# Kernel optimization log

Hardware: AMD Instinct MI355X
Metric: run time of the kernel (lower is better)

Reference implementation:

```python
import jax, jax.numpy as jnp
import numpy as np

B, T, D, N = 16, 4096, 512, 3


def _window_sum(x, k):
    # x: [B, T, ...] -> sliding-window sum of size k, stride 1 -> [B, T-k+1, ...]
    c = jnp.cumsum(x, axis=1)
    c = jnp.concatenate([jnp.zeros_like(c[:, :1]), c], axis=1)
    return c[:, k:] - c[:, :-k]


def setup_inputs() -> dict:
    key = jax.random.key(0)
    ks = jax.random.split(key, 7)
    s_prev = jax.random.normal(ks[0], (B, D), jnp.float32)
    enc_hs = jax.random.normal(ks[1], (B, T, D), jnp.float32)
    # realistic padding mask: True = padded position
    lengths = jax.random.randint(ks[2], (B,), T // 2, T + 1)
    src_mask = jnp.arange(T)[None, :] >= lengths[:, None]
    scale = 1.0 / np.sqrt(D)
    Vw = jax.random.normal(ks[3], (N, D, D), jnp.float32) * scale
    Vb = jax.random.normal(ks[4], (N, D), jnp.float32) * 0.01
    Ww = jax.random.normal(ks[5], (N, D, D), jnp.float32) * scale
    Wb = jax.random.normal(ks[6], (N, D), jnp.float32) * 0.01
    return {"s_prev": s_prev, "enc_hs": enc_hs, "src_mask": src_mask,
            "Vw": Vw, "Vb": Vb, "Ww": Ww, "Wb": Wb}


def _level(s_prev, hs, mask, vw, vb, ww, wb):
    # hs: [B, L, D], mask: [B, L] (True = masked)
    # torch Linear: y = x @ W^T + b, weight is [out, in]
    v = jnp.einsum('bld,ed->ble', hs, vw) + vb            # V_i(hs)
    att = jnp.einsum('bd,bld->bl', s_prev, v)             # bmm(s_prev, V(hs)^T)
    att = jnp.where(mask, -jnp.inf, att)
    att = jax.nn.softmax(att, axis=-1)                    # [B, L]
    pooled = jnp.einsum('bl,bld->bd', att, hs)            # bmm(att, hs)
    ctx = pooled @ ww.T + wb                              # W_i(.)
    return ctx, att


def reference(s_prev, enc_hs, src_mask, Vw, Vb, Ww, Wb):
    ctx, att = _level(s_prev, enc_hs, src_mask, Vw[0], Vb[0], Ww[0], Wb[0])
    for i in range(1, N):
        k = i + 1
        hs_ngram = _window_sum(enc_hs, k) / k                      # AvgPool1d(k,1)
        n_mask = _window_sum(src_mask.astype(jnp.float32), k) > 0  # any masked in window
        c, _ = _level(s_prev, hs_ngram, n_mask, Vw[i], Vb[i], Ww[i], Wb[i])
        ctx = ctx + c
    return ctx, att
```

## Files before the change

### kernel.cpp

```cpp
#include <hip/hip_runtime.h>

#define BB 16
#define TT 4096
#define DD 512
#define CH 32
#define NY (TT/CH)
#define NEG (-1.0e30f)

#define OFF_Q     64
#define OFF_P0    (OFF_Q + 3*BB*DD)
#define OFF_M     (OFF_P0 + BB*TT)
#define OFF_S     (OFF_M + 3*BB*NY)
#define OFF_MT    (OFF_S + 3*BB*NY)
#define OFF_TOT   (OFF_MT + 64)
#define OFF_PART  (OFF_TOT + 64)
#define OFF_POOL  (OFF_PART + 3*NY*BB*DD)

__global__ void __launch_bounds__(256) k_lengths(const unsigned char* __restrict__ mask,
                                                 int* __restrict__ lengths) {
    __shared__ int sflag;
    __shared__ int wsum[4];
    const int tid = threadIdx.x;
    const int b = blockIdx.x;
    if (tid == 0) sflag = 0;
    __syncthreads();
    const uint4* m4 = (const uint4*)mask;
    int f = 0;
    #pragma unroll 4
    for (int idx = tid; idx < BB * TT / 16; idx += 256) {
        const uint4 w = m4[idx];
        f |= (((w.x | w.y | w.z | w.w) & 0xFFFFFF00u) != 0u);
    }
    if (f) atomicOr(&sflag, 1);
    __syncthreads();
    const bool byte_layout = (sflag != 0);
    const int* m32 = (const int*)mask;
    int cnt = 0;
    if (byte_layout) {
        for (int t = tid; t < TT; t += 256) cnt += (mask[b * TT + t] != 0);
    } else {
        for (int t = tid; t < TT; t += 256) cnt += (m32[b * TT + t] != 0);
    }
    #pragma unroll
    for (int m = 32; m >= 1; m >>= 1) cnt += __shfl_xor(cnt, m, 64);
    if ((tid & 63) == 0) wsum[tid >> 6] = cnt;
    __syncthreads();
    if (tid == 0) lengths[b] = TT - (wsum[0] + wsum[1] + wsum[2] + wsum[3]);
}

__global__ void __launch_bounds__(1024) k_q(const float* __restrict__ s_prev,
                                            const float* __restrict__ Vw,
                                            float* __restrict__ q) {
    __shared__ float red[4][DD];
    const int ib = blockIdx.x;
    const int b = ib % BB;
    const int i = ib / BB;
    const int ec = threadIdx.x >> 8;
    const int d0 = threadIdx.x & 255;
    const float* sp = s_prev + b * DD + ec * 128;
    const float* W = Vw + (size_t)i * DD * DD + (size_t)(ec * 128) * DD;
    float a0 = 0.f, a1 = 0.f;
    #pragma unroll 4
    for (int e = 0; e < 128; e++) {
        const float se = sp[e];
        a0 += se * W[e * DD + d0];
        a1 += se * W[e * DD + d0 + 256];
    }
    red[ec][d0] = a0;
    red[ec][d0 + 256] = a1;
    __syncthreads();
    if (threadIdx.x < DD)
        q[(size_t)ib * DD + threadIdx.x] = red[0][threadIdx.x] + red[1][threadIdx.x]
                                         + red[2][threadIdx.x] + red[3][threadIdx.x];
}

__global__ void __launch_bounds__(512, 4) k_fused(const float* __restrict__ enc,
                                                  const float* __restrict__ q,
                                                  const int* __restrict__ lengths,
                                                  float* __restrict__ p0,
                                                  float* __restrict__ mbuf,
                                                  float* __restrict__ sbuf,
                                                  float* __restrict__ part) {
    __shared__ float se[CH + 2][DD];
    __shared__ float sp[CH + 2][3];
    __shared__ float su[3][CH];
    const int b = blockIdx.x;
    const int y = blockIdx.y;
    const int t0 = y * CH;
    const int len = lengths[b];
    const int tid = threadIdx.x;
    if (t0 >= len) {
        if (tid < 3) {
            mbuf[(size_t)(tid * BB + b) * NY + y] = NEG;
            sbuf[(size_t)(tid * BB + b) * NY + y] = 0.f;
        }
        return;
    }
    const int wv = tid >> 6, lane = tid & 63;

    const float4* q40 = (const float4*)(q + (size_t)(0 * BB + b) * DD);
    const float4* q41 = (const float4*)(q + (size_t)(1 * BB + b) * DD);
    const float4* q42 = (const float4*)(q + (size_t)(2 * BB + b) * DD);
    const float4 qa0 = q40[lane], qb0 = q40[64 + lane];
    const float4 qa1 = q41[lane], qb1 = q41[64 + lane];
    const float4 qa2 = q42[lane], qb2 = q42[64 + lane];

    auto row_task = [&](const int r, const bool wp0) {
        const int t = t0 + r;
        float4 x0 = make_float4(0.f, 0.f, 0.f, 0.f), x1 = x0;
        if (t < TT) {
            const float4* e4 = (const float4*)(enc + ((size_t)b * TT + t) * DD);
            x0 = e4[lane]; x1 = e4[64 + lane];
        }
        ((float4*)se[r])[lane] = x0;
        ((float4*)se[r])[64 + lane] = x1;
        float d0 = x0.x*qa0.x + x0.y*qa0.y + x0.z*qa0.z + x0.w*qa0.w
                 + x1.x*qb0.x + x1.y*qb0.y + x1.z*qb0.z + x1.w*qb0.w;
        float d1 = x0.x*qa1.x + x0.y*qa1.y + x0.z*qa1.z + x0.w*qa1.w
                 + x1.x*qb1.x + x1.y*qb1.y + x1.z*qb1.z + x1.w*qb1.w;
        float d2 = x0.x*qa2.x + x0.y*qa2.y + x0.z*qa2.z + x0.w*qa2.w
                 + x1.x*qb2.x + x1.y*qb2.y + x1.z*qb2.z + x1.w*qb2.w;
        #pragma unroll
        for (int m = 32; m >= 1; m >>= 1) {
            d0 += __shfl_xor(d0, m, 64);
            d1 += __shfl_xor(d1, m, 64);
            d2 += __shfl_xor(d2, m, 64);
        }
        if (lane == 0) {
            sp[r][0] = d0; sp[r][1] = d1; sp[r][2] = d2;
            if (wp0 && t < TT) p0[(size_t)b * TT + t] = d0;
        }
    };
    #pragma unroll
    for (int rr = 0; rr < 4; rr++) row_task(wv + rr * 8, true);
    if (wv < 2) row_task(CH + wv, false);
    __syncthreads();

    if (tid < 192) {
        const int i = wv;
        const bool act = lane < CH;
        const int r = lane & (CH - 1);
        const int l = t0 + r;
        const bool valid = act && (l < (len - i));
        float v = NEG;
        if (act) {
            float s = sp[r][i];
            if (i > 0) s += sp[r + 1][i];
            if (i > 1) s += sp[r + 2][i];
            const float kin = (i == 0) ? 1.0f : ((i == 1) ? 0.5f : (1.0f / 3.0f));
            v = valid ? s * kin : NEG;
        }
        float m = v;
        #pragma unroll
        for (int mm = 32; mm >= 1; mm >>= 1) m = fmaxf(m, __shfl_xor(m, mm, 64));
        const float u = valid ? __expf(v - m) : 0.f;
        if (act) su[i][r] = u;
        float ts = u;
        #pragma unroll
        for (int mm = 32; mm >= 1; mm >>= 1) ts += __shfl_xor(ts, mm, 64);
        if (lane == 0) {
            mbuf[(size_t)(i * BB + b) * NY + y] = m;
            sbuf[(size_t)(i * BB + b) * NY + y] = ts;
        }
    }
    __syncthreads();

    float va = se[0][tid], vb2 = se[1][tid];
    float a0 = 0.f, a1 = 0.f, a2 = 0.f;
    #pragma unroll
    for (int g = 0; g < CH / 4; g++) {
        const float4 U0 = *(const float4*)&su[0][g * 4];
        const float4 U1 = *(const float4*)&su[1][g * 4];
        const float4 U2 = *(const float4*)&su[2][g * 4];
        const float u0a[4] = {U0.x, U0.y, U0.z, U0.w};
        const float u1a[4] = {U1.x, U1.y, U1.z, U1.w};
        const float u2a[4] = {U2.x, U2.y, U2.z, U2.w};
        #pragma unroll
        for (int j = 0; j < 4; j++) {
            const float vc = se[g * 4 + j + 2][tid];
            const float w1 = va + vb2;
            const float w2 = w1 + vc;
            a0 += u0a[j] * va;
            a1 += u1a[j] * w1;
            a2 += u2a[j] * w2;
            va = vb2; vb2 = vc;
        }
    }
    a1 *= 0.5f; a2 *= (1.0f / 3.0f);
    float* pt = part + (size_t)y * BB * DD + (size_t)b * DD + tid;
    pt[0] = a0;
    pt[(size_t)NY * BB * DD] = a1;
    pt[(size_t)2 * NY * BB * DD] = a2;
}

__global__ void __launch_bounds__(256) k_reduce(const float* __restrict__ part,
                                                const float* __restrict__ mbuf,
                                                const float* __restrict__ sbuf,
                                                float* __restrict__ pooled,
                                                float* __restrict__ mtot,
                                                float* __restrict__ tot) {
    __shared__ float ssc[NY];
    const int blk = blockIdx.x;
    const int ib = blk >> 1;
    const int d = ((blk & 1) << 8) + threadIdx.x;
    const int i = ib / BB, b = ib % BB;
    if (threadIdx.x < 64) {
        const int lane = threadIdx.x;
        float ml[2], sl[2];
        float m = NEG;
        #pragma unroll
        for (int j = 0; j < 2; j++) {
            ml[j] = mbuf[(size_t)ib * NY + lane * 2 + j];
            sl[j] = sbuf[(size_t)ib * NY + lane * 2 + j];
            m = fmaxf(m, ml[j]);
        }
        #pragma unroll
        for (int s = 32; s >= 1; s >>= 1) m = fmaxf(m, __shfl_xor(m, s, 64));
        float t = 0.f;
        #pragma unroll
        for (int j = 0; j < 2; j++) t += sl[j] * __expf(ml[j] - m);
        #pragma unroll
        for (int s = 32; s >= 1; s >>= 1) t += __shfl_xor(t, s, 64);
        const float inv = 1.0f / t;
        #pragma unroll
        for (int j = 0; j < 2; j++)
            ssc[lane * 2 + j] = __expf(ml[j] - m) * inv;
        if (lane == 0 && (blk & 1) == 0) { mtot[ib] = m; tot[ib] = t; }
    }
    __syncthreads();
    const float* base = part + (size_t)i * NY * BB * DD + (size_t)b * DD + d;
    float s = 0.f;
    #pragma unroll 8
    for (int yy = 0; yy < NY; yy++) s += base[(size_t)yy * BB * DD] * ssc[yy];
    pooled[(size_t)ib * DD + d] = s;
}

__global__ void __launch_bounds__(256) k_out(const float* __restrict__ pooled,
                                             const float* __restrict__ Ww,
                                             const float* __restrict__ Wb,
                                             const float* __restrict__ p0,
                                             const int* __restrict__ lengths,
                                             const float* __restrict__ mtot,
                                             const float* __restrict__ tot,
                                             float* __restrict__ ctx,
                                             float* __restrict__ att) {
    if (blockIdx.x < BB * DD / 4) {
        const int wid = blockIdx.x * 4 + (threadIdx.x >> 6);
        const int lane = threadIdx.x & 63;
        const int b = wid >> 9;
        const int e = wid & 511;
        float acc = 0.f;
        #pragma unroll
        for (int i = 0; i < 3; i++) {
            const float4* pr = (const float4*)(pooled + (size_t)(i * BB + b) * DD);
            const float4* wr = (const float4*)(Ww + ((size_t)i * DD + e) * DD);
            const float4 pA = pr[lane], pB = pr[64 + lane];
            const float4 wA = wr[lane], wB = wr[64 + lane];
            acc += pA.x * wA.x + pA.y * wA.y + pA.z * wA.z + pA.w * wA.w
                 + pB.x * wB.x + pB.y * wB.y + pB.z * wB.z + pB.w * wB.w;
        }
        #pragma unroll
        for (int m = 32; m >= 1; m >>= 1) acc += __shfl_xor(acc, m, 64);
        if (lane == 0)
            ctx[(size_t)b * DD + e] = acc + Wb[e] + Wb[DD + e] + Wb[2 * DD + e];
    } else {
        const int idx = (blockIdx.x - BB * DD / 4) * 256 + threadIdx.x;
        const int b = idx >> 12;
        const int t = idx & (TT - 1);
        att[idx] = (t < lengths[b]) ? __expf(p0[idx] - mtot[b]) * (1.0f / tot[b]) : 0.f;
    }
}

extern "C" void kernel_launch(void* const* d_in, const int* in_sizes, int n_in,
                              void* d_out, int out_size, void* d_ws, size_t ws_size,
                              hipStream_t stream) {
    const float* s_prev = (const float*)d_in[0];
    const float* enc    = (const float*)d_in[1];
    const void*  mask   = d_in[2];
    const float* Vw     = (const float*)d_in[3];
    const float* Ww     = (const float*)d_in[5];
    const float* Wb     = (const float*)d_in[6];

    float* out = (float*)d_out;
    float* ctx = out;
    float* att = out + BB * DD;

    float* W       = (float*)d_ws;
    int*   lengths = (int*)d_ws;
    float* q       = W + OFF_Q;
    float* p0      = W + OFF_P0;
    float* mbuf    = W + OFF_M;
    float* sbuf    = W + OFF_S;
    float* mtot    = W + OFF_MT;
    float* tot     = W + OFF_TOT;
    float* part    = W + OFF_PART;
    float* pooled  = W + OFF_POOL;

    k_lengths<<<BB, 256, 0, stream>>>((const unsigned char*)mask, lengths);
    k_q<<<48, 1024, 0, stream>>>(s_prev, Vw, q);
    k_fused<<<dim3(BB, NY), 512, 0, stream>>>(enc, q, lengths, p0, mbuf, sbuf, part);
    k_reduce<<<96, 256, 0, stream>>>(part, mbuf, sbuf, pooled, mtot, tot);
    k_out<<<BB * DD / 4 + BB * TT / 256, 256, 0, stream>>>(pooled, Ww, Wb, p0, lengths,
                                                           mtot, tot, ctx, att);
}
```

Baseline: 251.3 us.

## Process four chunks per block with online softmax and split q projection

Each fused block now walks four consecutive 32-row chunks and merges their partial softmax statistics and weighted sums with an online rescale. This cuts the number of per-chunk partials written to and read back from global memory by four, and shrinks the reduction kernel's work. The q projection is split across many more blocks, merged into the length kernel, with a small extra kernel to sum the pieces, so more CUs work on that stage. The trade-offs are fewer fused blocks (less parallelism and poorer tail balance), one extra launch, and extra barriers inside each block.

```diff
diff --git a/kernel.cpp b/kernel.cpp
--- a/kernel.cpp
+++ b/kernel.cpp
@@ -4,74 +4,94 @@
 #define TT 4096
 #define DD 512
 #define CH 32
-#define NY (TT/CH)
+#define GR 4
+#define NG (TT/(CH*GR))
 #define NEG (-1.0e30f)
 
 #define OFF_Q     64
-#define OFF_P0    (OFF_Q + 3*BB*DD)
+#define OFF_QP    (OFF_Q + 3*BB*DD)
+#define OFF_P0    (OFF_QP + 8*3*BB*DD)
 #define OFF_M     (OFF_P0 + BB*TT)
-#define OFF_S     (OFF_M + 3*BB*NY)
-#define OFF_MT    (OFF_S + 3*BB*NY)
+#define OFF_S     (OFF_M + 3*BB*NG)
+#define OFF_MT    (OFF_S + 3*BB*NG)
 #define OFF_TOT   (OFF_MT + 64)
 #define OFF_PART  (OFF_TOT + 64)
-#define OFF_POOL  (OFF_PART + 3*NY*BB*DD)
-
-__global__ void __launch_bounds__(256) k_lengths(const unsigned char* __restrict__ mask,
-                                                 int* __restrict__ lengths) {
-    __shared__ int sflag;
-    __shared__ int wsum[4];
+#define OFF_POOL  (OFF_PART + 3*NG*BB*DD)
+
+__global__ void __launch_bounds__(256) k_pre(const unsigned char* __restrict__ mask,
+                                             const float* __restrict__ s_prev,
+                                             const float* __restrict__ Vw,
+                                             int* __restrict__ lengths,
+                                             float* __restrict__ qpart) {
     const int tid = threadIdx.x;
-    const int b = blockIdx.x;
-    if (tid == 0) sflag = 0;
-    __syncthreads();
-    const uint4* m4 = (const uint4*)mask;
-    int f = 0;
-    #pragma unroll 4
-    for (int idx = tid; idx < BB * TT / 16; idx += 256) {
-        const uint4 w = m4[idx];
-        f |= (((w.x | w.y | w.z | w.w) & 0xFFFFFF00u) != 0u);
-    }
-    if (f) atomicOr(&sflag, 1);
-    __syncthreads();
-    const bool byte_layout = (sflag != 0);
-    const int* m32 = (const int*)mask;
-    int cnt = 0;
-    if (byte_layout) {
-        for (int t = tid; t < TT; t += 256) cnt += (mask[b * TT + t] != 0);
+    if (blockIdx.x < BB) {
+        __shared__ int sflag;
+        __shared__ int wsum[4];
+        const int b = blockIdx.x;
+        if (tid == 0) sflag = 0;
+        __syncthreads();
+        const uint4* m4 = (const uint4*)mask;
+        int f = 0;
+        #pragma unroll 4
+        for (int idx = tid; idx < BB * TT / 16; idx += 256) {
+            const uint4 w = m4[idx];
+            f |= (((w.x | w.y | w.z | w.w) & 0xFFFFFF00u) != 0u);
+        }
+        if (f) atomicOr(&sflag, 1);
+        __syncthreads();
+        const bool byte_layout = (sflag != 0);
+        const int* m32 = (const int*)mask;
+        int cnt = 0;
+        if (byte_layout) {
+            for (int t = tid; t < TT; t += 256) cnt += (mask[b * TT + t] != 0);
+        } else {
+            for (int t = tid; t < TT; t += 256) cnt += (m32[b * TT + t] != 0);
+        }
+        #pragma unroll
+        for (int m = 32; m >= 1; m >>= 1) cnt += __shfl_xor(cnt, m, 64);
+        if ((tid & 63) == 0) wsum[tid >> 6] = cnt;
+        __syncthreads();
+        if (tid == 0) lengths[b] = TT - (wsum[0] + wsum[1] + wsum[2] + wsum[3]);
     } else {
-        for (int t = tid; t < TT; t += 256) cnt += (m32[b * TT + t] != 0);
-    }
+        __shared__ float4 red[2][128];
+        const int idx = blockIdx.x - BB;
+        const int ib = idx >> 3;
+        const int ec = idx & 7;
+        const int b = ib % BB;
+        const int i = ib / BB;
+        const int es = tid >> 7;
+        const int dq = tid & 127;
+        const int e0 = ec * 64 + es * 32;
+        const float* sp = s_prev + b * DD + e0;
+        const float4* W = (const float4*)(Vw + (size_t)i * DD * DD + (size_t)e0 * DD) + dq;
+        float4 acc = make_float4(0.f, 0.f, 0.f, 0.f);
+        #pragma unroll 8
+        for (int e = 0; e < 32; e++) {
+            const float sev = sp[e];
+            const float4 w = W[e * 128];
+            acc.x += sev * w.x; acc.y += sev * w.y;
+            acc.z += sev * w.z; acc.w += sev * w.w;
+        }
+        red[es][dq] = acc;
+        __syncthreads();
+        if (tid < 128) {
+            const float4 r0 = red[0][tid], r1 = red[1][tid];
+            const float4 o = make_float4(r0.x + r1.x, r0.y + r1.y,
+                                         r0.z + r1.z, r0.w + r1.w);
+            ((float4*)(qpart + (size_t)idx * DD))[tid] = o;
+        }
+    }
+}
+
+__global__ void __launch_bounds__(256) k_q2(const float* __restrict__ qpart,
+                                            float* __restrict__ q) {
+    const int idx = blockIdx.x * 256 + threadIdx.x;
+    const int ib = idx / DD;
+    const int d = idx % DD;
+    float s = 0.f;
     #pragma unroll
-    for (int m = 32; m >= 1; m >>= 1) cnt += __shfl_xor(cnt, m, 64);
-    if ((tid & 63) == 0) wsum[tid >> 6] = cnt;
-    __syncthreads();
-    if (tid == 0) lengths[b] = TT - (wsum[0] + wsum[1] + wsum[2] + wsum[3]);
-}
-
-__global__ void __launch_bounds__(1024) k_q(const float* __restrict__ s_prev,
-                                            const float* __restrict__ Vw,
-                                            float* __restrict__ q) {
-    __shared__ float red[4][DD];
-    const int ib = blockIdx.x;
-    const int b = ib % BB;
-    const int i = ib / BB;
-    const int ec = threadIdx.x >> 8;
-    const int d0 = threadIdx.x & 255;
-    const float* sp = s_prev + b * DD + ec * 128;
-    const float* W = Vw + (size_t)i * DD * DD + (size_t)(ec * 128) * DD;
-    float a0 = 0.f, a1 = 0.f;
-    #pragma unroll 4
-    for (int e = 0; e < 128; e++) {
-        const float se = sp[e];
-        a0 += se * W[e * DD + d0];
-        a1 += se * W[e * DD + d0 + 256];
-    }
-    red[ec][d0] = a0;
-    red[ec][d0 + 256] = a1;
-    __syncthreads();
-    if (threadIdx.x < DD)
-        q[(size_t)ib * DD + threadIdx.x] = red[0][threadIdx.x] + red[1][threadIdx.x]
-                                         + red[2][threadIdx.x] + red[3][threadIdx.x];
+    for (int ec = 0; ec < 8; ec++) s += qpart[(size_t)(ib * 8 + ec) * DD + d];
+    q[idx] = s;
 }
 
 __global__ void __launch_bounds__(512, 4) k_fused(const float* __restrict__ enc,
@@ -84,15 +104,16 @@
     __shared__ float se[CH + 2][DD];
     __shared__ float sp[CH + 2][3];
     __shared__ float su[3][CH];
+    __shared__ float sms[3], sss[3];
     const int b = blockIdx.x;
-    const int y = blockIdx.y;
-    const int t0 = y * CH;
+    const int g = blockIdx.y;
+    const int t0g = g * (CH * GR);
     const int len = lengths[b];
     const int tid = threadIdx.x;
-    if (t0 >= len) {
+    if (t0g >= len) {
         if (tid < 3) {
-            mbuf[(size_t)(tid * BB + b) * NY + y] = NEG;
-            sbuf[(size_t)(tid * BB + b) * NY + y] = 0.f;
+            mbuf[(size_t)(tid * BB + b) * NG + g] = NEG;
+            sbuf[(size_t)(tid * BB + b) * NG + g] = 0.f;
         }
         return;
     }
@@ -105,92 +126,122 @@
     const float4 qa1 = q41[lane], qb1 = q41[64 + lane];
     const float4 qa2 = q42[lane], qb2 = q42[64 + lane];
 
-    auto row_task = [&](const int r, const bool wp0) {
-        const int t = t0 + r;
-        float4 x0 = make_float4(0.f, 0.f, 0.f, 0.f), x1 = x0;
-        if (t < TT) {
-            const float4* e4 = (const float4*)(enc + ((size_t)b * TT + t) * DD);
-            x0 = e4[lane]; x1 = e4[64 + lane];
-        }
-        ((float4*)se[r])[lane] = x0;
-        ((float4*)se[r])[64 + lane] = x1;
-        float d0 = x0.x*qa0.x + x0.y*qa0.y + x0.z*qa0.z + x0.w*qa0.w
-                 + x1.x*qb0.x + x1.y*qb0.y + x1.z*qb0.z + x1.w*qb0.w;
-        float d1 = x0.x*qa1.x + x0.y*qa1.y + x0.z*qa1.z + x0.w*qa1.w
-                 + x1.x*qb1.x + x1.y*qb1.y + x1.z*qb1.z + x1.w*qb1.w;
-        float d2 = x0.x*qa2.x + x0.y*qa2.y + x0.z*qa2.z + x0.w*qa2.w
-                 + x1.x*qb2.x + x1.y*qb2.y + x1.z*qb2.z + x1.w*qb2.w;
-        #pragma unroll
-        for (int m = 32; m >= 1; m >>= 1) {
-            d0 += __shfl_xor(d0, m, 64);
-            d1 += __shfl_xor(d1, m, 64);
-            d2 += __shfl_xor(d2, m, 64);
-        }
-        if (lane == 0) {
-            sp[r][0] = d0; sp[r][1] = d1; sp[r][2] = d2;
-            if (wp0 && t < TT) p0[(size_t)b * TT + t] = d0;
-        }
-    };
-    #pragma unroll
-    for (int rr = 0; rr < 4; rr++) row_task(wv + rr * 8, true);
-    if (wv < 2) row_task(CH + wv, false);
-    __syncthreads();
-
-    if (tid < 192) {
-        const int i = wv;
-        const bool act = lane < CH;
-        const int r = lane & (CH - 1);
-        const int l = t0 + r;
-        const bool valid = act && (l < (len - i));
-        float v = NEG;
-        if (act) {
-            float s = sp[r][i];
-            if (i > 0) s += sp[r + 1][i];
-            if (i > 1) s += sp[r + 2][i];
-            const float kin = (i == 0) ? 1.0f : ((i == 1) ? 0.5f : (1.0f / 3.0f));
-            v = valid ? s * kin : NEG;
-        }
-        float m = v;
-        #pragma unroll
-        for (int mm = 32; mm >= 1; mm >>= 1) m = fmaxf(m, __shfl_xor(m, mm, 64));
-        const float u = valid ? __expf(v - m) : 0.f;
-        if (act) su[i][r] = u;
-        float ts = u;
-        #pragma unroll
-        for (int mm = 32; mm >= 1; mm >>= 1) ts += __shfl_xor(ts, mm, 64);
-        if (lane == 0) {
-            mbuf[(size_t)(i * BB + b) * NY + y] = m;
-            sbuf[(size_t)(i * BB + b) * NY + y] = ts;
-        }
-    }
-    __syncthreads();
-
-    float va = se[0][tid], vb2 = se[1][tid];
-    float a0 = 0.f, a1 = 0.f, a2 = 0.f;
-    #pragma unroll
-    for (int g = 0; g < CH / 4; g++) {
-        const float4 U0 = *(const float4*)&su[0][g * 4];
-        const float4 U1 = *(const float4*)&su[1][g * 4];
-        const float4 U2 = *(const float4*)&su[2][g * 4];
-        const float u0a[4] = {U0.x, U0.y, U0.z, U0.w};
-        const float u1a[4] = {U1.x, U1.y, U1.z, U1.w};
-        const float u2a[4] = {U2.x, U2.y, U2.z, U2.w};
-        #pragma unroll
-        for (int j = 0; j < 4; j++) {
-            const float vc = se[g * 4 + j + 2][tid];
-            const float w1 = va + vb2;
-            const float w2 = w1 + vc;
-            a0 += u0a[j] * va;
-            a1 += u1a[j] * w1;
-            a2 += u2a[j] * w2;
-            va = vb2; vb2 = vc;
-        }
-    }
-    a1 *= 0.5f; a2 *= (1.0f / 3.0f);
-    float* pt = part + (size_t)y * BB * DD + (size_t)b * DD + tid;
-    pt[0] = a0;
-    pt[(size_t)NY * BB * DD] = a1;
-    pt[(size_t)2 * NY * BB * DD] = a2;
+    float M0 = NEG, M1 = NEG, M2 = NEG;
+    float S0 = 0.f, S1 = 0.f, S2 = 0.f;
+    float A0 = 0.f, A1 = 0.f, A2 = 0.f;
+
+    for (int sub = 0; sub < GR; sub++) {
+        const int t0 = t0g + sub * CH;
+        if (t0 >= len) break;
+        if (sub) __syncthreads();
+
+        auto row_task = [&](const int r, const bool wp0) {
+            const int t = t0 + r;
+            float4 x0 = make_float4(0.f, 0.f, 0.f, 0.f), x1 = x0;
+            if (t < TT) {
+                const float4* e4 = (const float4*)(enc + ((size_t)b * TT + t) * DD);
+                x0 = e4[lane]; x1 = e4[64 + lane];
+            }
+            ((float4*)se[r])[lane] = x0;
+            ((float4*)se[r])[64 + lane] = x1;
+            float d0 = x0.x*qa0.x + x0.y*qa0.y + x0.z*qa0.z + x0.w*qa0.w
+                     + x1.x*qb0.x + x1.y*qb0.y + x1.z*qb0.z + x1.w*qb0.w;
+            float d1 = x0.x*qa1.x + x0.y*qa1.y + x0.z*qa1.z + x0.w*qa1.w
+                     + x1.x*qb1.x + x1.y*qb1.y + x1.z*qb1.z + x1.w*qb1.w;
+            float d2 = x0.x*qa2.x + x0.y*qa2.y + x0.z*qa2.z + x0.w*qa2.w
+                     + x1.x*qb2.x + x1.y*qb2.y + x1.z*qb2.z + x1.w*qb2.w;
+            #pragma unroll
+            for (int m = 32; m >= 1; m >>= 1) {
+                d0 += __shfl_xor(d0, m, 64);
+                d1 += __shfl_xor(d1, m, 64);
+                d2 += __shfl_xor(d2, m, 64);
+            }
+            if (lane == 0) {
+                sp[r][0] = d0; sp[r][1] = d1; sp[r][2] = d2;
+                if (wp0 && t < TT) p0[(size_t)b * TT + t] = d0;
+            }
+        };
+        #pragma unroll
+        for (int rr = 0; rr < 4; rr++) row_task(wv + rr * 8, true);
+        if (wv < 2) row_task(CH + wv, false);
+        __syncthreads();
+
+        if (tid < 192) {
+            const int i = wv;
+            const bool act = lane < CH;
+            const int r = lane & (CH - 1);
+            const int l = t0 + r;
+            const bool valid = act && (l < (len - i));
+            float v = NEG;
+            if (act) {
+                float s = sp[r][i];
+                if (i > 0) s += sp[r + 1][i];
+                if (i > 1) s += sp[r + 2][i];
+                const float kin = (i == 0) ? 1.0f : ((i == 1) ? 0.5f : (1.0f / 3.0f));
+                v = valid ? s * kin : NEG;
+            }
+            float m = v;
+            #pragma unroll
+            for (int mm = 32; mm >= 1; mm >>= 1) m = fmaxf(m, __shfl_xor(m, mm, 64));
+            const float u = valid ? __expf(v - m) : 0.f;
+            if (act) su[i][r] = u;
+            float ts = u;
+            #pragma unroll
+            for (int mm = 32; mm >= 1; mm >>= 1) ts += __shfl_xor(ts, mm, 64);
+            if (lane == 0) { sms[i] = m; sss[i] = ts; }
+        }
+        __syncthreads();
+
+        float va = se[0][tid], vb2 = se[1][tid];
+        float a0 = 0.f, a1 = 0.f, a2 = 0.f;
+        #pragma unroll
+        for (int gg = 0; gg < CH / 4; gg++) {
+            const float4 U0 = *(const float4*)&su[0][gg * 4];
+            const float4 U1 = *(const float4*)&su[1][gg * 4];
+            const float4 U2 = *(const float4*)&su[2][gg * 4];
+            const float u0a[4] = {U0.x, U0.y, U0.z, U0.w};
+            const float u1a[4] = {U1.x, U1.y, U1.z, U1.w};
+            const float u2a[4] = {U2.x, U2.y, U2.z, U2.w};
+            #pragma unroll
+            for (int j = 0; j < 4; j++) {
+                const float vc = se[gg * 4 + j + 2][tid];
+                const float w1 = va + vb2;
+                const float w2 = w1 + vc;
+                a0 += u0a[j] * va;
+                a1 += u1a[j] * w1;
+                a2 += u2a[j] * w2;
+                va = vb2; vb2 = vc;
+            }
+        }
+        const float m0j = sms[0], m1j = sms[1], m2j = sms[2];
+        const float s0j = sss[0], s1j = sss[1], s2j = sss[2];
+        {
+            const float nM = fmaxf(M0, m0j);
+            const float so = __expf(M0 - nM), sn = __expf(m0j - nM);
+            A0 = A0 * so + a0 * sn;  S0 = S0 * so + s0j * sn;  M0 = nM;
+        }
+        {
+            const float nM = fmaxf(M1, m1j);
+            const float so = __expf(M1 - nM), sn = __expf(m1j - nM);
+            A1 = A1 * so + a1 * sn;  S1 = S1 * so + s1j * sn;  M1 = nM;
+        }
+        {
+            const float nM = fmaxf(M2, m2j);
+            const float so = __expf(M2 - nM), sn = __expf(m2j - nM);
+            A2 = A2 * so + a2 * sn;  S2 = S2 * so + s2j * sn;  M2 = nM;
+        }
+    }
+    A1 *= 0.5f; A2 *= (1.0f / 3.0f);
+    float* pt = part + (size_t)g * BB * DD + (size_t)b * DD + tid;
+    pt[0] = A0;
+    pt[(size_t)NG * BB * DD] = A1;
+    pt[(size_t)2 * NG * BB * DD] = A2;
+    if (tid < 3) {
+        const float Mv = (tid == 0) ? M0 : ((tid == 1) ? M1 : M2);
+        const float Sv = (tid == 0) ? S0 : ((tid == 1) ? S1 : S2);
+        mbuf[(size_t)(tid * BB + b) * NG + g] = Mv;
+        sbuf[(size_t)(tid * BB + b) * NG + g] = Sv;
+    }
 }
 
 __global__ void __launch_bounds__(256) k_reduce(const float* __restrict__ part,
@@ -199,39 +250,35 @@
                                                 float* __restrict__ pooled,
                                                 float* __restrict__ mtot,
                                                 float* __restrict__ tot) {
-    __shared__ float ssc[NY];
+    __shared__ float ssc[NG];
     const int blk = blockIdx.x;
     const int ib = blk >> 1;
     const int d = ((blk & 1) << 8) + threadIdx.x;
     const int i = ib / BB, b = ib % BB;
     if (threadIdx.x < 64) {
         const int lane = threadIdx.x;
-        float ml[2], sl[2];
-        float m = NEG;
-        #pragma unroll
-        for (int j = 0; j < 2; j++) {
-            ml[j] = mbuf[(size_t)ib * NY + lane * 2 + j];
-            sl[j] = sbuf[(size_t)ib * NY + lane * 2 + j];
-            m = fmaxf(m, ml[j]);
-        }
+        const bool a = lane < NG;
+        const float ml = a ? mbuf[(size_t)ib * NG + lane] : NEG;
+        const float sl = a ? sbuf[(size_t)ib * NG + lane] : 0.f;
+        float m = ml;
         #pragma unroll
         for (int s = 32; s >= 1; s >>= 1) m = fmaxf(m, __shfl_xor(m, s, 64));
-        float t = 0.f;
-        #pragma unroll
-        for (int j = 0; j < 2; j++) t += sl[j] * __expf(ml[j] - m);
+        float t = sl * __expf(ml - m);
         #pragma unroll
         for (int s = 32; s >= 1; s >>= 1) t += __shfl_xor(t, s, 64);
         const float inv = 1.0f / t;
-        #pragma unroll
-        for (int j = 0; j < 2; j++)
-            ssc[lane * 2 + j] = __expf(ml[j] - m) * inv;
+        if (a) ssc[lane] = __expf(ml - m) * inv;
         if (lane == 0 && (blk & 1) == 0) { mtot[ib] = m; tot[ib] = t; }
     }
     __syncthreads();
-    const float* base = part + (size_t)i * NY * BB * DD + (size_t)b * DD + d;
+    const float* base = part + (size_t)i * NG * BB * DD + (size_t)b * DD + d;
     float s = 0.f;
-    #pragma unroll 8
-    for (int yy = 0; yy < NY; yy++) s += base[(size_t)yy * BB * DD] * ssc[yy];
+    #pragma unroll
+    for (int yy = 0; yy < NG; yy++) {
+        const float sc = ssc[yy];
+        const float v = (sc != 0.f) ? base[(size_t)yy * BB * DD] : 0.f;
+        s += v * sc;
+    }
     pooled[(size_t)ib * DD + d] = s;
 }
 
@@ -288,6 +335,7 @@
     float* W       = (float*)d_ws;
     int*   lengths = (int*)d_ws;
     float* q       = W + OFF_Q;
+    float* qpart   = W + OFF_QP;
     float* p0      = W + OFF_P0;
     float* mbuf    = W + OFF_M;
     float* sbuf    = W + OFF_S;
@@ -296,9 +344,10 @@
     float* part    = W + OFF_PART;
     float* pooled  = W + OFF_POOL;
 
-    k_lengths<<<BB, 256, 0, stream>>>((const unsigned char*)mask, lengths);
-    k_q<<<48, 1024, 0, stream>>>(s_prev, Vw, q);
-    k_fused<<<dim3(BB, NY), 512, 0, stream>>>(enc, q, lengths, p0, mbuf, sbuf, part);
+    k_pre<<<BB + 48 * 8, 256, 0, stream>>>((const unsigned char*)mask, s_prev, Vw,
+                                           lengths, qpart);
+    k_q2<<<3 * BB * DD / 256, 256, 0, stream>>>(qpart, q);
+    k_fused<<<dim3(BB, NG), 512, 0, stream>>>(enc, q, lengths, p0, mbuf, sbuf, part);
     k_reduce<<<96, 256, 0, stream>>>(part, mbuf, sbuf, pooled, mtot, tot);
     k_out<<<BB * DD / 4 + BB * TT / 256, 256, 0, stream>>>(pooled, Ww, Wb, p0, lengths,
                                                            mtot, tot, ctx, att);
```

Measured after the change: 227.7 us. -9.4%, faster.
